# Performance work log

Hardware: AMD Instinct MI355X
Metric: run time of the kernel (lower is better)

## Reference

```python
import jax, jax.numpy as jnp
import numpy as np
import math

DIM_Q = 512; DIM_K = 512; DIM_V = 512; H = 8; EPS = 1e-5

def _layernorm(x, g, b):
    mu = jnp.mean(x, axis=-1, keepdims=True)
    var = jnp.mean((x - mu) ** 2, axis=-1, keepdims=True)
    return (x - mu) * jax.lax.rsqrt(var + EPS) * g + b

def setup_inputs() -> dict:
    key = jax.random.key(0)
    ks = jax.random.split(key, 12)
    B, NQ, NK = 8, 1024, 1024
    s = 0.02
    return {
        "Q": jax.random.normal(ks[0], (B, NQ, DIM_Q), jnp.float32),
        "K": jax.random.normal(ks[1], (B, NK, DIM_K), jnp.float32),
        "attention_mask": jax.random.randint(ks[2], (B, NK), 0, 2, jnp.int32),
        "Wq": jax.random.normal(ks[3], (DIM_Q, DIM_V), jnp.float32) * s,
        "bq": jnp.zeros((DIM_V,), jnp.float32),
        "Wk": jax.random.normal(ks[4], (DIM_K, DIM_V), jnp.float32) * s,
        "bk": jnp.zeros((DIM_V,), jnp.float32),
        "Wv": jax.random.normal(ks[5], (DIM_K, DIM_V), jnp.float32) * s,
        "bv": jnp.zeros((DIM_V,), jnp.float32),
        "Wo": jax.random.normal(ks[6], (DIM_V, DIM_V), jnp.float32) * s,
        "bo": jnp.zeros((DIM_V,), jnp.float32),
        "g0": jnp.ones((DIM_V,), jnp.float32),
        "b0": jnp.zeros((DIM_V,), jnp.float32),
        "g1": jnp.ones((DIM_V,), jnp.float32),
        "b1": jnp.zeros((DIM_V,), jnp.float32),
    }

def reference(Q, K, attention_mask, Wq, bq, Wk, bk, Wv, bv, Wo, bo, g0, b0, g1, b1):
    B, NQ, _ = Q.shape
    NK = K.shape[1]
    dh = DIM_V // H
    q = (Q @ Wq + bq).reshape(B, NQ, H, dh).transpose(0, 2, 1, 3)  # (B,H,NQ,dh)
    k = (K @ Wk + bk).reshape(B, NK, H, dh).transpose(0, 2, 1, 3)
    v = (K @ Wv + bv).reshape(B, NK, H, dh).transpose(0, 2, 1, 3)
    # NOTE: original scales by sqrt(dim_V), not sqrt(head_dim)
    scores = jnp.einsum("bhqd,bhkd->bhqk", q, k) / math.sqrt(DIM_V)
    scores = jnp.where(attention_mask[:, None, None, :] == 0, -10000.0, scores)
    A = jax.nn.softmax(scores, axis=-1)
    o = q + jnp.einsum("bhqk,bhkd->bhqd", A, v)  # residual before output proj
    O = o.transpose(0, 2, 1, 3).reshape(B, NQ, DIM_V)
    O = _layernorm(O, g0, b0)
    O = O + jax.nn.relu(O @ Wo + bo)
    O = _layernorm(O, g1, b1)
    return O
```

## Files before the change

kernel.cpp:

```cpp
#include <hip/hip_runtime.h>
#include <hip/hip_bf16.h>

typedef __attribute__((ext_vector_type(8))) short short8;
typedef __attribute__((ext_vector_type(4))) short short4v;
typedef __attribute__((ext_vector_type(4))) float float4v;
typedef __attribute__((ext_vector_type(4))) unsigned uint4v;

#define LDK 72
#define SCALE2 0.06376540791556074f
#define MBIAS2 -14426.950408889634f
#define PCLAMP 12.0f
#define EPS 76

__device__ inline unsigned short f2b(float f) {
    return __builtin_bit_cast(unsigned short, __float2bfloat16(f));
}
__device__ inline float b2f(unsigned short s) {
    return __uint_as_float(((unsigned)s) << 16);
}
__device__ inline unsigned pk2(float lo, float hi) {
    return (unsigned)f2b(lo) | ((unsigned)f2b(hi) << 16);
}
__device__ __forceinline__ void gld16(const unsigned short* g, unsigned short* l) {
    __builtin_amdgcn_global_load_lds(
        (const __attribute__((address_space(1))) void*)g,
        (__attribute__((address_space(3))) void*)l, 16, 0, 0);
}

__global__ void cast_bf16_kernel(const float* __restrict__ in,
                                 unsigned short* __restrict__ out, int n) {
    int i = (blockIdx.x * blockDim.x + threadIdx.x) * 8;
    if (i < n) {
        float4v a = *(const float4v*)(in + i);
        float4v b = *(const float4v*)(in + i + 4);
        uint4v o = {pk2(a[0], a[1]), pk2(a[2], a[3]), pk2(b[0], b[1]), pk2(b[2], b[3])};
        *(uint4v*)(out + i) = o;
    }
}

__global__ void transpose_w_kernel(const float* __restrict__ W0, const float* __restrict__ W1,
                                   const float* __restrict__ W2, const float* __restrict__ W3,
                                   unsigned short* __restrict__ out) {
    const float* W = (blockIdx.z == 0) ? W0 : (blockIdx.z == 1) ? W1
                   : (blockIdx.z == 2) ? W2 : W3;
    unsigned short* o = out + (size_t)blockIdx.z * 512 * 512;
    __shared__ float tile[32][33];
    int k0 = blockIdx.x * 32, n0 = blockIdx.y * 32;
    int tx = threadIdx.x & 31, ty = threadIdx.x >> 5;
    for (int r = ty; r < 32; r += 8) tile[r][tx] = W[(size_t)(k0 + r) * 512 + n0 + tx];
    __syncthreads();
    for (int r = ty; r < 32; r += 8) o[(size_t)(n0 + r) * 512 + k0 + tx] = f2b(tile[tx][r]);
}

__global__ __launch_bounds__(256) void gemm_kernel(
    const unsigned short* __restrict__ Qb, const unsigned short* __restrict__ Kb,
    const unsigned short* __restrict__ hb, const unsigned short* __restrict__ WT,
    const float* __restrict__ bq, const float* __restrict__ bk,
    const float* __restrict__ bv, const float* __restrict__ bo,
    unsigned short* __restrict__ qo, unsigned short* __restrict__ ko,
    unsigned short* __restrict__ vTo, unsigned short* __restrict__ to_,
    int zbase) {
    int z = zbase + blockIdx.z;
    const unsigned short* A = (z == 0) ? Qb : (z == 3) ? hb : Kb;
    const unsigned short* BT = WT + (size_t)z * 512 * 512;
    const float* bias = (z == 0) ? bq : (z == 1) ? bk : (z == 2) ? bv : bo;

    __shared__ unsigned short SM[4][8192];

    int tid = threadIdx.x;
    int lane = tid & 63, wave = tid >> 6;
    int wr = wave >> 1, wc = wave & 1;
    int l15 = lane & 15, lg = lane >> 4;
    int row0 = blockIdx.x * 128, col0 = blockIdx.y * 128;

    float4v acc[4][4];
#pragma unroll
    for (int m = 0; m < 4; m++)
#pragma unroll
        for (int n = 0; n < 4; n++) acc[m][n] = (float4v){0.f, 0.f, 0.f, 0.f};

    int srow = wave * 32 + (lane >> 3);
    int gch = (lane & 7) ^ (srow & 7);
    const unsigned short* gA = A + (size_t)(row0 + srow) * 512 + gch * 8;
    const unsigned short* gB = BT + (size_t)(col0 + srow) * 512 + gch * 8;
    int sw = l15 & 7;

    auto STAGE = [&](int bi, int t) {
        unsigned short* lA = SM[bi * 2] + wave * 2048;
        unsigned short* lB = SM[bi * 2 + 1] + wave * 2048;
        int k0 = t * 64;
#pragma unroll
        for (int c = 0; c < 4; c++) {
            gld16(gA + (size_t)c * 4096 + k0, lA + c * 512);
            gld16(gB + (size_t)c * 4096 + k0, lB + c * 512);
        }
    };
    auto COMPUTE = [&](int bi) {
        const unsigned short* As = SM[bi * 2];
        const unsigned short* Bs = SM[bi * 2 + 1];
#pragma unroll
        for (int kk = 0; kk < 2; kk++) {
            int ck = ((kk * 4 + lg) ^ sw) * 8;
            short8 af[4], bf[4];
#pragma unroll
            for (int m = 0; m < 4; m++)
                af[m] = *(const short8*)(As + (wr * 64 + m * 16 + l15) * 64 + ck);
#pragma unroll
            for (int n = 0; n < 4; n++)
                bf[n] = *(const short8*)(Bs + (wc * 64 + n * 16 + l15) * 64 + ck);
#pragma unroll
            for (int m = 0; m < 4; m++)
#pragma unroll
                for (int n = 0; n < 4; n++)
                    acc[m][n] = __builtin_amdgcn_mfma_f32_16x16x32_bf16(af[m], bf[n], acc[m][n], 0, 0, 0);
        }
    };

    STAGE(0, 0);
    __syncthreads();
    int buf = 0;
    for (int t = 0; t < 7; t++) {
        STAGE(buf ^ 1, t + 1);
        COMPUTE(buf);
        __syncthreads();
        buf ^= 1;
    }
    COMPUTE(buf);

    if (z == 2) {
#pragma unroll
        for (int n = 0; n < 4; n++) {
            int col = col0 + wc * 64 + n * 16 + l15;
            float bias_v = bias[col];
            int h = col >> 6, d = col & 63;
#pragma unroll
            for (int m = 0; m < 4; m++) {
                int rowb = row0 + wr * 64 + m * 16 + lg * 4;
                int b = rowb >> 10, tq = rowb & 1023;
                float4v v = acc[m][n];
                short4v st;
#pragma unroll
                for (int r = 0; r < 4; r++) st[r] = (short)f2b(v[r] + bias_v);
                *(short4v*)(vTo + ((((size_t)b * 8 + h) * 64 + d) << 10) + tq) = st;
            }
        }
    } else {
        __syncthreads();
        unsigned short* ep = &SM[0][0] + wave * (64 * EPS);
#pragma unroll
        for (int n = 0; n < 4; n++) {
            float bias_v = bias[col0 + wc * 64 + n * 16 + l15];
#pragma unroll
            for (int m = 0; m < 4; m++) {
                float4v v = acc[m][n];
#pragma unroll
                for (int r = 0; r < 4; r++) {
                    float x = v[r] + bias_v;
                    if (z == 3) x = x > 0.f ? x : 0.f;
                    ep[(m * 16 + lg * 4 + r) * EPS + n * 16 + l15] = f2b(x);
                }
            }
        }
        int lr = lane >> 3, lc = lane & 7;
        unsigned short* o = (z == 0) ? qo : (z == 1) ? ko : to_;
#pragma unroll
        for (int p = 0; p < 8; p++) {
            int row_l = p * 8 + lr;
            short8 vv = *(const short8*)(ep + row_l * EPS + lc * 8);
            size_t gidx = (size_t)(row0 + wr * 64 + row_l) * 512 + col0 + wc * 64 + lc * 8;
            if (z == 3) {
                short8 hv = *(const short8*)(hb + gidx);
                short8 o8;
#pragma unroll
                for (int j = 0; j < 8; j++)
                    o8[j] = (short)f2b(b2f((unsigned short)vv[j]) + b2f((unsigned short)hv[j]));
                *(short8*)(o + gidx) = o8;
            } else {
                *(short8*)(o + gidx) = vv;
            }
        }
    }
}

__global__ __launch_bounds__(256) void attn_kernel(
    const unsigned short* __restrict__ qb, const unsigned short* __restrict__ kb,
    const unsigned short* __restrict__ vT, const int* __restrict__ mask,
    unsigned short* __restrict__ ob) {
    __shared__ unsigned short Ks[2][64 * LDK];
    __shared__ unsigned short Vs[2][64 * LDK];
    __shared__ float mb[2][64];

    int tid = threadIdx.x;
    int lane = tid & 63, wave = tid >> 6;
    int l15 = lane & 15, lg = lane >> 4;
    int bh = blockIdx.y;
    int b = bh >> 3, h = bh & 7;
    int qrow0 = b * 1024 + blockIdx.x * 64 + wave * 16;

    short8 qf[2];
#pragma unroll
    for (int kk = 0; kk < 2; kk++)
        qf[kk] = *(const short8*)(qb + (size_t)(qrow0 + l15) * 512 + h * 64 + kk * 32 + lg * 8);

    float l_acc = 0.f;
    float4v oacc[4];
#pragma unroll
    for (int n = 0; n < 4; n++) oacc[n] = (float4v){0.f, 0.f, 0.f, 0.f};

    int srow = tid >> 2, soff = (tid & 2) * 16;
    int shalf = (tid & 1) * 16;
    int koff = soff + shalf;
    int prow = (srow & 0x23) | ((srow & 4) << 2) | ((srow & 0x18) >> 1);

    short8 kreg[2], vreg[2];
    int mreg = 0;
    auto LOADR = [&](int t) {
        const unsigned short* kg = kb + (size_t)(b * 1024 + t * 64 + srow) * 512 + h * 64 + koff;
        kreg[0] = *(const short8*)kg;
        kreg[1] = *(const short8*)(kg + 8);
        const unsigned short* vg = vT + (((size_t)bh * 64 + srow) << 10) + t * 64 + koff;
        vreg[0] = *(const short8*)vg;
        vreg[1] = *(const short8*)(vg + 8);
        if (tid < 64) mreg = mask[b * 1024 + t * 64 + tid];
    };
    auto WLDS = [&](int bi) {
        *(short8*)(Ks[bi] + prow * LDK + koff) = kreg[0];
        *(short8*)(Ks[bi] + prow * LDK + koff + 8) = kreg[1];
        *(short8*)(Vs[bi] + srow * LDK + koff) = vreg[0];
        *(short8*)(Vs[bi] + srow * LDK + koff + 8) = vreg[1];
        if (tid < 64) mb[bi][tid] = mreg ? 0.f : MBIAS2;
    };

    LOADR(0);
    WLDS(0);
    __syncthreads();
    int buf = 0;
    for (int t = 0; t < 16; t++) {
        if (t < 15) LOADR(t + 1);

        const unsigned short* Kc = Ks[buf];
        const unsigned short* Vc = Vs[buf];
        float p[4][4];
#pragma unroll
        for (int jf = 0; jf < 4; jf++) {
            short8 kf0 = *(const short8*)(Kc + (jf * 16 + l15) * LDK + lg * 8);
            short8 kf1 = *(const short8*)(Kc + (jf * 16 + l15) * LDK + 32 + lg * 8);
            float4v tt = (float4v){0.f, 0.f, 0.f, 0.f};
            tt = __builtin_amdgcn_mfma_f32_16x16x32_bf16(kf0, qf[0], tt, 0, 0, 0);
            tt = __builtin_amdgcn_mfma_f32_16x16x32_bf16(kf1, qf[1], tt, 0, 0, 0);
#pragma unroll
            for (int r = 0; r < 4; r++) p[jf][r] = tt[r];
        }
#pragma unroll
        for (int jf = 0; jf < 4; jf++)
#pragma unroll
            for (int r = 0; r < 4; r++) {
                float val = fminf(fmaf(p[jf][r], SCALE2,
                                       mb[buf][32 * (jf >> 1) + 8 * lg + 4 * (jf & 1) + r]),
                                  PCLAMP);
                float e = exp2f(val);
                p[jf][r] = e;
                l_acc += e;
            }
        short8 pb[2];
#pragma unroll
        for (int ks = 0; ks < 2; ks++) {
            uint4v w = {pk2(p[2 * ks][0], p[2 * ks][1]), pk2(p[2 * ks][2], p[2 * ks][3]),
                        pk2(p[2 * ks + 1][0], p[2 * ks + 1][1]),
                        pk2(p[2 * ks + 1][2], p[2 * ks + 1][3])};
            pb[ks] = __builtin_bit_cast(short8, w);
        }
#pragma unroll
        for (int n = 0; n < 4; n++)
#pragma unroll
            for (int ks = 0; ks < 2; ks++) {
                short8 vf = *(const short8*)(Vc + (n * 16 + l15) * LDK + ks * 32 + lg * 8);
                oacc[n] = __builtin_amdgcn_mfma_f32_16x16x32_bf16(vf, pb[ks], oacc[n], 0, 0, 0);
            }

        if (t < 15) {
            WLDS(buf ^ 1);
            __syncthreads();
            buf ^= 1;
        }
    }

    l_acc += __shfl_xor(l_acc, 16);
    l_acc += __shfl_xor(l_acc, 32);
    float inv = 1.f / l_acc;
#pragma unroll
    for (int n = 0; n < 4; n++) {
        size_t base = (size_t)(qrow0 + l15) * 512 + h * 64 + n * 16 + lg * 4;
        short4v qr = *(const short4v*)(qb + base);
        short4v st;
#pragma unroll
        for (int r = 0; r < 4; r++)
            st[r] = (short)f2b(b2f((unsigned short)qr[r]) + oacc[n][r] * inv);
        *(short4v*)(ob + base) = st;
    }
}

__global__ void ln_kernel_bf16(const unsigned short* __restrict__ in,
                               const float* __restrict__ g, const float* __restrict__ bb,
                               unsigned short* __restrict__ out) {
    int row = blockIdx.x, lane = threadIdx.x;
    short8 v = *(const short8*)(in + (size_t)row * 512 + lane * 8);
    float x[8], s = 0.f, s2 = 0.f;
#pragma unroll
    for (int j = 0; j < 8; j++) {
        x[j] = b2f((unsigned short)v[j]);
        s += x[j];
        s2 += x[j] * x[j];
    }
#pragma unroll
    for (int off = 1; off < 64; off <<= 1) {
        s += __shfl_xor(s, off);
        s2 += __shfl_xor(s2, off);
    }
    float mu = s * (1.f / 512.f);
    float var = s2 * (1.f / 512.f) - mu * mu;
    float rs = rsqrtf(var + 1e-5f);
#pragma unroll
    for (int j = 0; j < 8; j++) {
        int c = lane * 8 + j;
        out[(size_t)row * 512 + c] = f2b((x[j] - mu) * rs * g[c] + bb[c]);
    }
}

__global__ void ln_kernel_f32(const unsigned short* __restrict__ in,
                              const float* __restrict__ g, const float* __restrict__ bb,
                              float* __restrict__ out) {
    int row = blockIdx.x, lane = threadIdx.x;
    short8 v = *(const short8*)(in + (size_t)row * 512 + lane * 8);
    float x[8], s = 0.f, s2 = 0.f;
#pragma unroll
    for (int j = 0; j < 8; j++) {
        x[j] = b2f((unsigned short)v[j]);
        s += x[j];
        s2 += x[j] * x[j];
    }
#pragma unroll
    for (int off = 1; off < 64; off <<= 1) {
        s += __shfl_xor(s, off);
        s2 += __shfl_xor(s2, off);
    }
    float mu = s * (1.f / 512.f);
    float var = s2 * (1.f / 512.f) - mu * mu;
    float rs = rsqrtf(var + 1e-5f);
#pragma unroll
    for (int j = 0; j < 8; j++) {
        int c = lane * 8 + j;
        out[(size_t)row * 512 + c] = (x[j] - mu) * rs * g[c] + bb[c];
    }
}

extern "C" void kernel_launch(void* const* d_in, const int* in_sizes, int n_in,
                              void* d_out, int out_size, void* d_ws, size_t ws_size,
                              hipStream_t stream) {
    const float* Q = (const float*)d_in[0];
    const float* K = (const float*)d_in[1];
    const int* mask = (const int*)d_in[2];
    const float* Wq = (const float*)d_in[3];
    const float* bq = (const float*)d_in[4];
    const float* Wk = (const float*)d_in[5];
    const float* bk = (const float*)d_in[6];
    const float* Wv = (const float*)d_in[7];
    const float* bv = (const float*)d_in[8];
    const float* Wo = (const float*)d_in[9];
    const float* bo = (const float*)d_in[10];
    const float* g0 = (const float*)d_in[11];
    const float* b0 = (const float*)d_in[12];
    const float* g1 = (const float*)d_in[13];
    const float* b1 = (const float*)d_in[14];
    float* out = (float*)d_out;

    const size_t N = 8192ull * 512;
    unsigned short* w16 = (unsigned short*)d_ws;
    unsigned short* Qb = w16;
    unsigned short* Kb = Qb + N;
    unsigned short* WT = Kb + N;
    unsigned short* qb = WT + 4ull * 512 * 512;
    unsigned short* kb = qb + N;
    unsigned short* vTb = kb + N;
    unsigned short* obuf = vTb + N;
    unsigned short* hbuf = obuf + N;
    unsigned short* tbuf = hbuf + N;

    cast_bf16_kernel<<<2048, 256, 0, stream>>>(Q, Qb, (int)N);
    cast_bf16_kernel<<<2048, 256, 0, stream>>>(K, Kb, (int)N);
    transpose_w_kernel<<<dim3(16, 16, 4), 256, 0, stream>>>(Wq, Wk, Wv, Wo, WT);
    gemm_kernel<<<dim3(64, 4, 3), 256, 0, stream>>>(Qb, Kb, hbuf, WT, bq, bk, bv, bo,
                                                    qb, kb, vTb, tbuf, 0);
    attn_kernel<<<dim3(16, 64), 256, 0, stream>>>(qb, kb, vTb, mask, obuf);
    ln_kernel_bf16<<<8192, 64, 0, stream>>>(obuf, g0, b0, hbuf);
    gemm_kernel<<<dim3(64, 4, 1), 256, 0, stream>>>(Qb, Kb, hbuf, WT, bq, bk, bv, bo,
                                                    qb, kb, vTb, tbuf, 3);
    ln_kernel_f32<<<8192, 64, 0, stream>>>(tbuf, g1, b1, out);
}
```

Baseline: 191.2 us.

## Use 8-wave GEMM tiles, XOR-swizzled attention LDS, merged cast, drop exp clamp

The GEMM moves to 512 threads (8 waves, each computing 64x32 instead of 64x64). Staging and the epilogue become block-wide, with a shared padded LDS tile for the coalesced store. The attention kernel replaces padded LDS rows with XOR-swizzled 64-wide rows, precomputes the mask bias at load time, and drops the fminf clamp before exp2. The two cast launches are merged into one, cutting launch overhead. These aim at latency hiding and LDS bank conflicts, at the cost of lower per-wave reuse in the GEMM and possible overflow from removing the clamp.

```diff
diff --git a/kernel.cpp b/kernel.cpp
--- a/kernel.cpp
+++ b/kernel.cpp
@@ -6,11 +6,9 @@
 typedef __attribute__((ext_vector_type(4))) float float4v;
 typedef __attribute__((ext_vector_type(4))) unsigned uint4v;
 
-#define LDK 72
 #define SCALE2 0.06376540791556074f
 #define MBIAS2 -14426.950408889634f
-#define PCLAMP 12.0f
-#define EPS 76
+#define EPST 136
 
 __device__ inline unsigned short f2b(float f) {
     return __builtin_bit_cast(unsigned short, __float2bfloat16(f));
@@ -27,15 +25,19 @@
         (__attribute__((address_space(3))) void*)l, 16, 0, 0);
 }
 
-__global__ void cast_bf16_kernel(const float* __restrict__ in,
-                                 unsigned short* __restrict__ out, int n) {
-    int i = (blockIdx.x * blockDim.x + threadIdx.x) * 8;
-    if (i < n) {
-        float4v a = *(const float4v*)(in + i);
-        float4v b = *(const float4v*)(in + i + 4);
-        uint4v o = {pk2(a[0], a[1]), pk2(a[2], a[3]), pk2(b[0], b[1]), pk2(b[2], b[3])};
-        *(uint4v*)(out + i) = o;
-    }
+__global__ void cast_bf16_kernel(const float* __restrict__ Q, const float* __restrict__ K,
+                                 unsigned short* __restrict__ Qb,
+                                 unsigned short* __restrict__ Kb, int n) {
+    int gid = blockIdx.x * blockDim.x + threadIdx.x;
+    int i = gid * 8;
+    const float* in;
+    unsigned short* out;
+    if (i < n) { in = Q + i; out = Qb + i; }
+    else       { in = K + (i - n); out = Kb + (i - n); }
+    float4v a = *(const float4v*)in;
+    float4v b = *(const float4v*)(in + 4);
+    uint4v o = {pk2(a[0], a[1]), pk2(a[2], a[3]), pk2(b[0], b[1]), pk2(b[2], b[3])};
+    *(uint4v*)out = o;
 }
 
 __global__ void transpose_w_kernel(const float* __restrict__ W0, const float* __restrict__ W1,
@@ -52,7 +54,7 @@
     for (int r = ty; r < 32; r += 8) o[(size_t)(n0 + r) * 512 + k0 + tx] = f2b(tile[tx][r]);
 }
 
-__global__ __launch_bounds__(256) void gemm_kernel(
+__global__ __launch_bounds__(512) void gemm_kernel(
     const unsigned short* __restrict__ Qb, const unsigned short* __restrict__ Kb,
     const unsigned short* __restrict__ hb, const unsigned short* __restrict__ WT,
     const float* __restrict__ bq, const float* __restrict__ bk,
@@ -69,30 +71,29 @@
 
     int tid = threadIdx.x;
     int lane = tid & 63, wave = tid >> 6;
-    int wr = wave >> 1, wc = wave & 1;
-    int l15 = lane & 15, lg = lane >> 4;
+    int wr = wave >> 2, wc = wave & 3;
+    int l15 = lane & 15, lg = lane >> 4, l7 = l15 & 7;
     int row0 = blockIdx.x * 128, col0 = blockIdx.y * 128;
 
-    float4v acc[4][4];
+    float4v acc[4][2];
 #pragma unroll
     for (int m = 0; m < 4; m++)
 #pragma unroll
-        for (int n = 0; n < 4; n++) acc[m][n] = (float4v){0.f, 0.f, 0.f, 0.f};
-
-    int srow = wave * 32 + (lane >> 3);
-    int gch = (lane & 7) ^ (srow & 7);
-    const unsigned short* gA = A + (size_t)(row0 + srow) * 512 + gch * 8;
-    const unsigned short* gB = BT + (size_t)(col0 + srow) * 512 + gch * 8;
-    int sw = l15 & 7;
+        for (int n = 0; n < 2; n++) acc[m][n] = (float4v){0.f, 0.f, 0.f, 0.f};
+
+    int sr8 = tid >> 3;
+    int gch = (tid & 7) ^ (sr8 & 7);
+    const unsigned short* gA0 = A + (size_t)(row0 + sr8) * 512 + gch * 8;
+    const unsigned short* gB0 = BT + (size_t)(col0 + sr8) * 512 + gch * 8;
 
     auto STAGE = [&](int bi, int t) {
-        unsigned short* lA = SM[bi * 2] + wave * 2048;
-        unsigned short* lB = SM[bi * 2 + 1] + wave * 2048;
         int k0 = t * 64;
-#pragma unroll
-        for (int c = 0; c < 4; c++) {
-            gld16(gA + (size_t)c * 4096 + k0, lA + c * 512);
-            gld16(gB + (size_t)c * 4096 + k0, lB + c * 512);
+        unsigned short* lA = SM[bi * 2] + wave * 512;
+        unsigned short* lB = SM[bi * 2 + 1] + wave * 512;
+#pragma unroll
+        for (int c = 0; c < 2; c++) {
+            gld16(gA0 + (size_t)c * 32768 + k0, lA + c * 4096);
+            gld16(gB0 + (size_t)c * 32768 + k0, lB + c * 4096);
         }
     };
     auto COMPUTE = [&](int bi) {
@@ -100,18 +101,18 @@
         const unsigned short* Bs = SM[bi * 2 + 1];
 #pragma unroll
         for (int kk = 0; kk < 2; kk++) {
-            int ck = ((kk * 4 + lg) ^ sw) * 8;
-            short8 af[4], bf[4];
+            int ck = ((kk * 4 + lg) ^ l7) * 8;
+            short8 af[4], bf[2];
 #pragma unroll
             for (int m = 0; m < 4; m++)
                 af[m] = *(const short8*)(As + (wr * 64 + m * 16 + l15) * 64 + ck);
 #pragma unroll
-            for (int n = 0; n < 4; n++)
-                bf[n] = *(const short8*)(Bs + (wc * 64 + n * 16 + l15) * 64 + ck);
+            for (int n = 0; n < 2; n++)
+                bf[n] = *(const short8*)(Bs + (wc * 32 + n * 16 + l15) * 64 + ck);
 #pragma unroll
             for (int m = 0; m < 4; m++)
 #pragma unroll
-                for (int n = 0; n < 4; n++)
+                for (int n = 0; n < 2; n++)
                     acc[m][n] = __builtin_amdgcn_mfma_f32_16x16x32_bf16(af[m], bf[n], acc[m][n], 0, 0, 0);
         }
     };
@@ -129,8 +130,8 @@
 
     if (z == 2) {
 #pragma unroll
-        for (int n = 0; n < 4; n++) {
-            int col = col0 + wc * 64 + n * 16 + l15;
+        for (int n = 0; n < 2; n++) {
+            int col = col0 + wc * 32 + n * 16 + l15;
             float bias_v = bias[col];
             int h = col >> 6, d = col & 63;
 #pragma unroll
@@ -146,10 +147,11 @@
         }
     } else {
         __syncthreads();
-        unsigned short* ep = &SM[0][0] + wave * (64 * EPS);
-#pragma unroll
-        for (int n = 0; n < 4; n++) {
-            float bias_v = bias[col0 + wc * 64 + n * 16 + l15];
+        unsigned short* ep = &SM[0][0];
+#pragma unroll
+        for (int n = 0; n < 2; n++) {
+            int cl = wc * 32 + n * 16 + l15;
+            float bias_v = bias[col0 + cl];
 #pragma unroll
             for (int m = 0; m < 4; m++) {
                 float4v v = acc[m][n];
@@ -157,17 +159,18 @@
                 for (int r = 0; r < 4; r++) {
                     float x = v[r] + bias_v;
                     if (z == 3) x = x > 0.f ? x : 0.f;
-                    ep[(m * 16 + lg * 4 + r) * EPS + n * 16 + l15] = f2b(x);
+                    ep[(wr * 64 + m * 16 + lg * 4 + r) * EPST + cl] = f2b(x);
                 }
             }
         }
-        int lr = lane >> 3, lc = lane & 7;
+        __syncthreads();
+        int rr = tid >> 4, cc = (tid & 15) * 8;
         unsigned short* o = (z == 0) ? qo : (z == 1) ? ko : to_;
 #pragma unroll
-        for (int p = 0; p < 8; p++) {
-            int row_l = p * 8 + lr;
-            short8 vv = *(const short8*)(ep + row_l * EPS + lc * 8);
-            size_t gidx = (size_t)(row0 + wr * 64 + row_l) * 512 + col0 + wc * 64 + lc * 8;
+        for (int p = 0; p < 4; p++) {
+            int row_l = p * 32 + rr;
+            short8 vv = *(const short8*)(ep + row_l * EPST + cc);
+            size_t gidx = (size_t)(row0 + row_l) * 512 + col0 + cc;
             if (z == 3) {
                 short8 hv = *(const short8*)(hb + gidx);
                 short8 o8;
@@ -186,13 +189,13 @@
     const unsigned short* __restrict__ qb, const unsigned short* __restrict__ kb,
     const unsigned short* __restrict__ vT, const int* __restrict__ mask,
     unsigned short* __restrict__ ob) {
-    __shared__ unsigned short Ks[2][64 * LDK];
-    __shared__ unsigned short Vs[2][64 * LDK];
+    __shared__ unsigned short Ks[2][64 * 64];
+    __shared__ unsigned short Vs[2][64 * 64];
     __shared__ float mb[2][64];
 
     int tid = threadIdx.x;
     int lane = tid & 63, wave = tid >> 6;
-    int l15 = lane & 15, lg = lane >> 4;
+    int l15 = lane & 15, lg = lane >> 4, l7 = l15 & 7;
     int bh = blockIdx.y;
     int b = bh >> 3, h = bh & 7;
     int qrow0 = b * 1024 + blockIdx.x * 64 + wave * 16;
@@ -207,13 +210,13 @@
 #pragma unroll
     for (int n = 0; n < 4; n++) oacc[n] = (float4v){0.f, 0.f, 0.f, 0.f};
 
-    int srow = tid >> 2, soff = (tid & 2) * 16;
-    int shalf = (tid & 1) * 16;
-    int koff = soff + shalf;
+    int srow = tid >> 2, koff = (tid & 3) * 16;
+    int kc0 = koff >> 3;
     int prow = (srow & 0x23) | ((srow & 4) << 2) | ((srow & 0x18) >> 1);
+    int pk = prow & 7, sk = srow & 7;
 
     short8 kreg[2], vreg[2];
-    int mreg = 0;
+    float mreg = 0.f;
     auto LOADR = [&](int t) {
         const unsigned short* kg = kb + (size_t)(b * 1024 + t * 64 + srow) * 512 + h * 64 + koff;
         kreg[0] = *(const short8*)kg;
@@ -221,14 +224,14 @@
         const unsigned short* vg = vT + (((size_t)bh * 64 + srow) << 10) + t * 64 + koff;
         vreg[0] = *(const short8*)vg;
         vreg[1] = *(const short8*)(vg + 8);
-        if (tid < 64) mreg = mask[b * 1024 + t * 64 + tid];
+        if (tid < 64) mreg = mask[b * 1024 + t * 64 + tid] ? 0.f : MBIAS2;
     };
     auto WLDS = [&](int bi) {
-        *(short8*)(Ks[bi] + prow * LDK + koff) = kreg[0];
-        *(short8*)(Ks[bi] + prow * LDK + koff + 8) = kreg[1];
-        *(short8*)(Vs[bi] + srow * LDK + koff) = vreg[0];
-        *(short8*)(Vs[bi] + srow * LDK + koff + 8) = vreg[1];
-        if (tid < 64) mb[bi][tid] = mreg ? 0.f : MBIAS2;
+        *(short8*)(Ks[bi] + prow * 64 + ((kc0 ^ pk) << 3))       = kreg[0];
+        *(short8*)(Ks[bi] + prow * 64 + (((kc0 + 1) ^ pk) << 3)) = kreg[1];
+        *(short8*)(Vs[bi] + srow * 64 + ((kc0 ^ sk) << 3))       = vreg[0];
+        *(short8*)(Vs[bi] + srow * 64 + (((kc0 + 1) ^ sk) << 3)) = vreg[1];
+        if (tid < 64) mb[bi][tid] = mreg;
     };
 
     LOADR(0);
@@ -243,8 +246,8 @@
         float p[4][4];
 #pragma unroll
         for (int jf = 0; jf < 4; jf++) {
-            short8 kf0 = *(const short8*)(Kc + (jf * 16 + l15) * LDK + lg * 8);
-            short8 kf1 = *(const short8*)(Kc + (jf * 16 + l15) * LDK + 32 + lg * 8);
+            short8 kf0 = *(const short8*)(Kc + (jf * 16 + l15) * 64 + ((lg ^ l7) << 3));
+            short8 kf1 = *(const short8*)(Kc + (jf * 16 + l15) * 64 + (((4 + lg) ^ l7) << 3));
             float4v tt = (float4v){0.f, 0.f, 0.f, 0.f};
             tt = __builtin_amdgcn_mfma_f32_16x16x32_bf16(kf0, qf[0], tt, 0, 0, 0);
             tt = __builtin_amdgcn_mfma_f32_16x16x32_bf16(kf1, qf[1], tt, 0, 0, 0);
@@ -255,10 +258,8 @@
         for (int jf = 0; jf < 4; jf++)
 #pragma unroll
             for (int r = 0; r < 4; r++) {
-                float val = fminf(fmaf(p[jf][r], SCALE2,
-                                       mb[buf][32 * (jf >> 1) + 8 * lg + 4 * (jf & 1) + r]),
-                                  PCLAMP);
-                float e = exp2f(val);
+                float e = exp2f(fmaf(p[jf][r], SCALE2,
+                                     mb[buf][32 * (jf >> 1) + 8 * lg + 4 * (jf & 1) + r]));
                 p[jf][r] = e;
                 l_acc += e;
             }
@@ -274,7 +275,7 @@
         for (int n = 0; n < 4; n++)
 #pragma unroll
             for (int ks = 0; ks < 2; ks++) {
-                short8 vf = *(const short8*)(Vc + (n * 16 + l15) * LDK + ks * 32 + lg * 8);
+                short8 vf = *(const short8*)(Vc + (n * 16 + l15) * 64 + (((ks * 4 + lg) ^ l7) << 3));
                 oacc[n] = __builtin_amdgcn_mfma_f32_16x16x32_bf16(vf, pb[ks], oacc[n], 0, 0, 0);
             }
 
@@ -386,14 +387,13 @@
     unsigned short* hbuf = obuf + N;
     unsigned short* tbuf = hbuf + N;
 
-    cast_bf16_kernel<<<2048, 256, 0, stream>>>(Q, Qb, (int)N);
-    cast_bf16_kernel<<<2048, 256, 0, stream>>>(K, Kb, (int)N);
+    cast_bf16_kernel<<<4096, 256, 0, stream>>>(Q, K, Qb, Kb, (int)N);
     transpose_w_kernel<<<dim3(16, 16, 4), 256, 0, stream>>>(Wq, Wk, Wv, Wo, WT);
-    gemm_kernel<<<dim3(64, 4, 3), 256, 0, stream>>>(Qb, Kb, hbuf, WT, bq, bk, bv, bo,
+    gemm_kernel<<<dim3(64, 4, 3), 512, 0, stream>>>(Qb, Kb, hbuf, WT, bq, bk, bv, bo,
                                                     qb, kb, vTb, tbuf, 0);
     attn_kernel<<<dim3(16, 64), 256, 0, stream>>>(qb, kb, vTb, mask, obuf);
     ln_kernel_bf16<<<8192, 64, 0, stream>>>(obuf, g0, b0, hbuf);
-    gemm_kernel<<<dim3(64, 4, 1), 256, 0, stream>>>(Qb, Kb, hbuf, WT, bq, bk, bv, bo,
+    gemm_kernel<<<dim3(64, 4, 1), 512, 0, stream>>>(Qb, Kb, hbuf, WT, bq, bk, bv, bo,
                                                     qb, kb, vTb, tbuf, 3);
     ln_kernel_f32<<<8192, 64, 0, stream>>>(tbuf, g1, b1, out);
 }
```

After: 195.4 us. 2.2% more time.
